# Kernel tuning notes

Hardware: AMD Instinct MI355X
Metric: run time of the kernel (lower is better)

Reference implementation:

```python
import jax, jax.numpy as jnp
import numpy as np

HIDDEN = 1024
NUM_HEADS = 16
B, S = 2, 2048


def _mha(x, w_in, b_in, w_out, b_out, num_heads):
    # x: [..., L, E]; standard nn.MultiheadAttention math (eval mode, no dropout)
    lead = x.shape[:-2]
    L, E = x.shape[-2], x.shape[-1]
    dh = E // num_heads
    qkv = x @ w_in.T + b_in                      # [..., L, 3E]
    q, k, v = jnp.split(qkv, 3, axis=-1)
    q = q.reshape(lead + (L, num_heads, dh)) * (dh ** -0.5)
    k = k.reshape(lead + (L, num_heads, dh))
    v = v.reshape(lead + (L, num_heads, dh))
    scores = jnp.einsum('...qhd,...khd->...hqk', q, k)
    probs = jax.nn.softmax(scores, axis=-1)
    out = jnp.einsum('...hqk,...khd->...qhd', probs, v).reshape(lead + (L, E))
    return out @ w_out.T + b_out


def setup_inputs() -> dict:
    key = jax.random.key(0)
    ks = jax.random.split(key, 12)
    E = HIDDEN
    s_in = 1.0 / np.sqrt(E)
    inp = {
        'x': jax.random.normal(ks[0], (B, S, E), dtype=jnp.float32),
        'w_in_g': jax.random.normal(ks[1], (3 * E, E), dtype=jnp.float32) * s_in,
        'b_in_g': jnp.zeros((3 * E,), dtype=jnp.float32),
        'w_out_g': jax.random.normal(ks[2], (E, E), dtype=jnp.float32) * s_in,
        'b_out_g': jnp.zeros((E,), dtype=jnp.float32),
        'w_in_l': jax.random.normal(ks[3], (3 * E, E), dtype=jnp.float32) * s_in,
        'b_in_l': jnp.zeros((3 * E,), dtype=jnp.float32),
        'w_out_l': jax.random.normal(ks[4], (E, E), dtype=jnp.float32) * s_in,
        'b_out_l': jnp.zeros((E,), dtype=jnp.float32),
        'w_f': jax.random.normal(ks[5], (E, 2 * E), dtype=jnp.float32) * (1.0 / np.sqrt(2 * E)),
        'b_f': jnp.zeros((E,), dtype=jnp.float32),
    }
    return inp


def reference(x, w_in_g, b_in_g, w_out_g, b_out_g,
              w_in_l, b_in_l, w_out_l, b_out_l, w_f, b_f):
    Bn, Sn, E = x.shape
    # global full attention over the whole sequence
    g = _mha(x, w_in_g, b_in_g, w_out_g, b_out_g, NUM_HEADS)   # [B,S,E]
    # block-local attention: blocks of length num_heads along the sequence
    sub_len = NUM_HEADS
    sub_num = Sn // sub_len
    xb = x.reshape(Bn, sub_num, sub_len, E)
    l = _mha(xb, w_in_l, b_in_l, w_out_l, b_out_l, NUM_HEADS).reshape(Bn, Sn, E)
    fused = jnp.concatenate([g, l], axis=-1)                   # [B,S,2E]
    return fused @ w_f.T + b_f
```

## Files before the change

### kernel.cpp

```cpp
#include <hip/hip_runtime.h>
#include <hip/hip_bf16.h>
#include <math.h>
#include <stdint.h>

constexpr int Bz = 2;
constexpr int S  = 2048;
constexpr int E  = 1024;
constexpr int NH = 16;
constexpr int DH = 64;
constexpr int QS = 6144;

typedef __attribute__((ext_vector_type(8))) short short8;
typedef __attribute__((ext_vector_type(4))) float f32x4;
typedef __attribute__((ext_vector_type(8))) unsigned short bf16x8;
typedef __attribute__((ext_vector_type(4))) unsigned short bf16x4;

__device__ __forceinline__ float bf2f(unsigned short u) {
    union { unsigned int i; float f; } c; c.i = ((unsigned int)u) << 16; return c.f;
}
__device__ __forceinline__ unsigned short f2bf(float f) {
    union { float f; unsigned int i; } c; c.f = f;
    unsigned int r = c.i + 0x7fffu + ((c.i >> 16) & 1u);
    return (unsigned short)(r >> 16);
}

__device__ __forceinline__ void pack4_store(unsigned short* dst,
                                            float a, float b, float c, float d) {
#if __has_builtin(__builtin_amdgcn_cvt_pk_bf16_f32)
    auto p0 = __builtin_amdgcn_cvt_pk_bf16_f32(a, b);
    auto p1 = __builtin_amdgcn_cvt_pk_bf16_f32(c, d);
    union { decltype(p0) v; unsigned int u; } c0, c1;
    c0.v = p0; c1.v = p1;
    uint2 w; w.x = c0.u; w.y = c1.u;
    *(uint2*)dst = w;
#else
    bf16x4 o = { f2bf(a), f2bf(b), f2bf(c), f2bf(d) };
    *(bf16x4*)dst = o;
#endif
}

#define GLD_LDS(g, l) __builtin_amdgcn_global_load_lds( \
    (const __attribute__((address_space(1))) void*)(g), \
    (__attribute__((address_space(3))) void*)(l), 16, 0, 0)

struct PrepArgs {
    const float* csrc[4]; unsigned short* cdst[4]; int cn[4];
    const float* wog; const float* wol;
    unsigned short* wogT; unsigned short* wolT;
    const float* wf; const float* bf; const float* bog; const float* bol;
    float* cb;
};

__global__ __launch_bounds__(256)
void prep_all(PrepArgs a)
{
    __shared__ unsigned short T[64][72];
    const int bid = blockIdx.x, t = threadIdx.x;

    if (bid < 12288) {
        int i = (bid * 256 + t) * 4;
        #pragma unroll
        for (int r = 0; r < 4; ++r) {
            if (i < a.cn[r]) {
                float4 v = *(const float4*)(a.csrc[r] + i);
                bf16x4 o = { f2bf(v.x), f2bf(v.y), f2bf(v.z), f2bf(v.w) };
                *(bf16x4*)(a.cdst[r] + i) = o;
                return;
            }
            i -= a.cn[r];
        }
        return;
    }
    if (bid < 12800) {
        const int id = bid - 12288;
        const int tj = id & 15, ti = (id >> 4) & 15, mat = id >> 8;
        const float* src = mat ? a.wol : a.wog;
        unsigned short* dst = mat ? a.wolT : a.wogT;
        #pragma unroll
        for (int r = 0; r < 4; ++r) {
            const int c = r * 256 + t;
            const int row = c >> 4, col4 = (c & 15) * 4;
            float4 v = *(const float4*)(src + (size_t)(ti * 64 + row) * 1024 + tj * 64 + col4);
            T[col4 + 0][row] = f2bf(v.x);
            T[col4 + 1][row] = f2bf(v.y);
            T[col4 + 2][row] = f2bf(v.z);
            T[col4 + 3][row] = f2bf(v.w);
        }
        __syncthreads();
        #pragma unroll
        for (int r = 0; r < 2; ++r) {
            const int c = r * 256 + t;
            const int jrow = c >> 3, ig = (c & 7) * 8;
            bf16x8 o;
            #pragma unroll
            for (int k = 0; k < 8; ++k) o[k] = T[jrow][ig + k];
            *(bf16x8*)(dst + (size_t)(tj * 64 + jrow) * 1024 + ti * 64 + ig) = o;
        }
        return;
    }
    {
        const int lane = t & 63;
        const int n = (bid - 12800) * 4 + (t >> 6);
        const float* row = a.wf + (size_t)n * 2048;
        float s = 0.f;
        #pragma unroll
        for (int i = 0; i < 16; ++i) s = fmaf(row[i * 64 + lane], a.bog[i * 64 + lane], s);
        #pragma unroll
        for (int i = 16; i < 32; ++i) s = fmaf(row[i * 64 + lane], a.bol[i * 64 + lane - 1024], s);
        #pragma unroll
        for (int off = 32; off > 0; off >>= 1) s += __shfl_xor(s, off, 64);
        if (lane == 0) a.cb[n] = a.bf[n] + s;
    }
}

struct GemmFusedArgs {
    const unsigned short* xb;    const unsigned short* win;
    const unsigned short* wfb;   const unsigned short* woutT;
    const float* bg;             const float* bl;
    unsigned short* qkv;  unsigned short* vt;  unsigned short* vtl;
    unsigned short* wcomb;
};

__global__ __launch_bounds__(256, 2)
void gemm_fused(GemmFusedArgs g)
{
    __shared__ __align__(16) short As[128 * 64];
    __shared__ __align__(16) short Bs[128 * 64];

    const int bid = blockIdx.x;
    const unsigned short *A, *W;
    unsigned short *C, *vt, *vtl;
    const float *bias0, *bias1;
    int m0, n0, lda, ldw, ldc, nsplit;

    if (bid < 1536) {
        m0 = (bid / 48) * 128;  n0 = (bid % 48) * 128;
        A = g.xb;  W = g.win;  C = g.qkv;  vt = g.vt;  vtl = g.vtl;
        bias0 = g.bg;  bias1 = g.bl;
        lda = 1024;  ldw = 1024;  ldc = QS;  nsplit = 3072;
    } else {
        const int id = bid - 1536;
        const int z = id >> 6;
        m0 = ((id >> 3) & 7) * 128;  n0 = (id & 7) * 128;
        A = g.wfb + z * 1024;
        W = g.woutT + (size_t)z * 1024 * 1024;
        C = g.wcomb + z * 1024;
        vt = nullptr;  vtl = nullptr;  bias0 = nullptr;  bias1 = nullptr;
        lda = 2048;  ldw = 1024;  ldc = 2048;  nsplit = 0;
    }

    const int t = threadIdx.x;
    const int lane = t & 63, wave = t >> 6;
    const int wm = wave & 1, wn = wave >> 1;
    const int lm = lane & 15, lk = lane >> 4;

    f32x4 acc[4][4] = {};

    const int row0 = t >> 3, kg0 = (t & 7) * 8;
    const unsigned short* a0 = A + (size_t)(m0 + row0) * lda + kg0;
    const unsigned short* w0 = W + (size_t)(n0 + row0) * ldw + kg0;

    for (int k0 = 0; k0 < 1024; k0 += 64) {
        __syncthreads();
        #pragma unroll
        for (int r = 0; r < 4; ++r)
            GLD_LDS(a0 + (size_t)(r * 32) * lda + k0, As + ((size_t)(r * 256 + wave * 64)) * 8);
        #pragma unroll
        for (int r = 0; r < 4; ++r)
            GLD_LDS(w0 + (size_t)(r * 32) * ldw + k0, Bs + ((size_t)(r * 256 + wave * 64)) * 8);
        __syncthreads();

        #pragma unroll
        for (int ks = 0; ks < 2; ++ks) {
            short8 af[4], bfr[4];
            #pragma unroll
            for (int i = 0; i < 4; ++i)
                af[i] = *(const short8*)&As[(wm * 64 + i * 16 + lm) * 64 + ks * 32 + lk * 8];
            #pragma unroll
            for (int j = 0; j < 4; ++j)
                bfr[j] = *(const short8*)&Bs[(wn * 64 + j * 16 + lm) * 64 + ks * 32 + lk * 8];
            #pragma unroll
            for (int i = 0; i < 4; ++i)
                #pragma unroll
                for (int j = 0; j < 4; ++j)
                    acc[i][j] = __builtin_amdgcn_mfma_f32_16x16x32_bf16(af[i], bfr[j], acc[i][j], 0, 0, 0);
        }
    }

    #pragma unroll
    for (int i = 0; i < 4; ++i) {
        #pragma unroll
        for (int j = 0; j < 4; ++j) {
            const int nn = n0 + wn * 64 + j * 16 + lm;
            const float bv = (nn < nsplit) ? (bias0 ? bias0[nn] : 0.f)
                                           : (bias1 ? bias1[nn - nsplit] : 0.f);
            const int mm0 = m0 + wm * 64 + i * 16 + lk * 4;
            float vv[4];
            #pragma unroll
            for (int r = 0; r < 4; ++r) {
                vv[r] = acc[i][j][r] + bv;
                C[(size_t)(mm0 + r) * ldc + nn] = f2bf(vv[r]);
            }
            if (vt) {
                const int nl = nn - 2048;
                if (nl >= 0 && nl < 1024) {
                    const int hh = nl >> 6, dd = nl & 63;
                    const int bb = mm0 >> 11, ss = mm0 & 2047;
                    pack4_store(vt + ((size_t)(bb * NH + hh) * 64 + dd) * S + ss,
                                vv[0], vv[1], vv[2], vv[3]);
                }
                const int nl2 = nn - 5120;
                if (nl2 >= 0) {
                    const int hh = nl2 >> 6, dd = nl2 & 63;
                    const int bb = mm0 >> 11, ss = mm0 & 2047;
                    pack4_store(vtl + ((size_t)(bb * NH + hh) * 64 + dd) * S + ss,
                                vv[0], vv[1], vv[2], vv[3]);
                }
            }
        }
    }
}

template<typename OutT>
__global__ __launch_bounds__(256, 2)
void gemm_m64(const unsigned short* __restrict__ A, const unsigned short* __restrict__ W,
              const float* __restrict__ bias, OutT* __restrict__ C,
              int M, int N, int K, int lda, int ldw, int ldc,
              size_t sAz, size_t sWz, size_t sCz)
{
    __shared__ __align__(16) short As[64 * 32];
    __shared__ __align__(16) short Bs[128 * 32];
    const int z = blockIdx.z;
    A += z * sAz;  W += z * sWz;  C += z * sCz;

    const int t = threadIdx.x;
    const int lane = t & 63, wave = t >> 6;
    const int wm = wave & 1, wn = wave >> 1;
    const int m0 = blockIdx.y * 64, n0 = blockIdx.x * 128;
    const int lm = lane & 15, lk = lane >> 4;

    f32x4 acc[2][4] = {};

    const int rowA = t >> 2, kgA = (t & 3) * 8;
    const unsigned short* aptr = A + (size_t)(m0 + rowA) * lda + kgA;
    const unsigned short* wptr = W + (size_t)(n0 + rowA) * ldw + kgA;

    for (int k0 = 0; k0 < K; k0 += 32) {
        __syncthreads();
        GLD_LDS(aptr + k0, As + ((size_t)(wave * 64)) * 8);
        #pragma unroll
        for (int r = 0; r < 2; ++r)
            GLD_LDS(wptr + (size_t)(r * 64) * ldw + k0, Bs + ((size_t)(r * 256 + wave * 64)) * 8);
        __syncthreads();

        short8 af[2], bfr[4];
        #pragma unroll
        for (int i = 0; i < 2; ++i)
            af[i] = *(const short8*)&As[(wm * 32 + i * 16 + lm) * 32 + lk * 8];
        #pragma unroll
        for (int j = 0; j < 4; ++j)
            bfr[j] = *(const short8*)&Bs[(wn * 64 + j * 16 + lm) * 32 + lk * 8];
        #pragma unroll
        for (int i = 0; i < 2; ++i)
            #pragma unroll
            for (int j = 0; j < 4; ++j)
                acc[i][j] = __builtin_amdgcn_mfma_f32_16x16x32_bf16(af[i], bfr[j], acc[i][j], 0, 0, 0);
    }

    #pragma unroll
    for (int i = 0; i < 2; ++i) {
        #pragma unroll
        for (int j = 0; j < 4; ++j) {
            const int nn = n0 + wn * 64 + j * 16 + lm;
            const float bv = bias ? bias[nn] : 0.f;
            #pragma unroll
            for (int r = 0; r < 4; ++r) {
                const int mm = m0 + wm * 32 + i * 16 + lk * 4 + r;
                const float v = acc[i][j][r] + bv;
                const size_t idx = (size_t)mm * ldc + nn;
                if constexpr (sizeof(OutT) == 2) ((unsigned short*)C)[idx] = f2bf(v);
                else                             C[idx] = v;
            }
        }
    }
}

__global__ __launch_bounds__(256, 2)
void attn_fused(const unsigned short* __restrict__ qkv,
                const unsigned short* __restrict__ vt,
                const unsigned short* __restrict__ vtl,
                unsigned short* __restrict__ attn)
{
    __shared__ __align__(16) unsigned short Ks[2][64][32];
    __shared__ __align__(16) unsigned short Vs[2][64][32];
    __shared__ __align__(16) unsigned short Pt[4][2][16][64];

    const int t = threadIdx.x, lane = t & 63, wq = t >> 6;
    const int lm = lane & 15, lk = lane >> 4;

    if (blockIdx.x < 512) {
        const int bid = blockIdx.x;
        const int qb = bid & 15;
        const int h  = (bid >> 4) & 15;
        const int b  = bid >> 8;
        const int q0 = qb * 128 + wq * 32;

        constexpr float QSCALE = 0.125f * 1.44269504088896340736f;
        short8 qf[2][2];
        #pragma unroll
        for (int qg = 0; qg < 2; ++qg) {
            const unsigned short* qrow = qkv + ((size_t)(b * S) + q0 + qg * 16 + lm) * QS + h * DH;
            #pragma unroll
            for (int kk = 0; kk < 2; ++kk) {
                bf16x8 v = *(const bf16x8*)(qrow + kk * 32 + lk * 8);
                #pragma unroll
                for (int j = 0; j < 8; ++j)
                    ((unsigned short*)&qf[qg][kk])[j] = f2bf(bf2f(v[j]) * QSCALE);
            }
        }

        short8 ones;
        #pragma unroll
        for (int j = 0; j < 8; ++j) ((unsigned short*)&ones)[j] = 0x3F80;

        const int row0 = t >> 2;
        const int sw0 = (row0 ^ (row0 >> 2)) & 3;
        const int g0 = ((t & 3) ^ sw0) * 8;
        const unsigned short* kg[2];
        const unsigned short* vg[2];
        #pragma unroll
        for (int r = 0; r < 2; ++r) {
            kg[r] = qkv + ((size_t)(b * S) + row0) * QS + E + h * 64 + r * 32 + g0;
            vg[r] = vt + ((size_t)(b * NH + h) * 64 + row0) * S + r * 32 + g0;
        }
        unsigned short* kl[2] = { &Ks[0][0][0] + (wq * 64) * 8, &Ks[0][0][0] + (256 + wq * 64) * 8 };
        unsigned short* vl[2] = { &Vs[0][0][0] + (wq * 64) * 8, &Vs[0][0][0] + (256 + wq * 64) * 8 };

        f32x4 O[2][4] = {};
        f32x4 lacc[2] = {};
        const int sw = lm & 7;
        const int fr = (lm ^ (lm >> 2)) & 3;

        for (int kt = 0; kt < 32; ++kt) {
            __syncthreads();
            GLD_LDS(kg[0] + (size_t)kt * 64 * QS, kl[0]);
            GLD_LDS(kg[1] + (size_t)kt * 64 * QS, kl[1]);
            GLD_LDS(vg[0] + kt * 64, vl[0]);
            GLD_LDS(vg[1] + kt * 64, vl[1]);
            __syncthreads();

            f32x4 st[2][4];
            #pragma unroll
            for (int qg = 0; qg < 2; ++qg)
                #pragma unroll
                for (int jn = 0; jn < 4; ++jn)
                    st[qg][jn] = (f32x4){ -16.f, -16.f, -16.f, -16.f };
            #pragma unroll
            for (int jn = 0; jn < 4; ++jn) {
                #pragma unroll
                for (int kk = 0; kk < 2; ++kk) {
                    short8 kf = *(const short8*)&Ks[kk][jn * 16 + lm][(lk ^ fr) * 8];
                    #pragma unroll
                    for (int qg = 0; qg < 2; ++qg)
                        st[qg][jn] = __builtin_amdgcn_mfma_f32_16x16x32_bf16(kf, qf[qg][kk], st[qg][jn], 0, 0, 0);
                }
            }

            #pragma unroll
            for (int qg = 0; qg < 2; ++qg)
                #pragma unroll
                for (int jn = 0; jn < 4; ++jn) {
                    const int cc = ((jn * 2 + (lk >> 1)) ^ sw) * 8 + (lk & 1) * 4;
                    pack4_store(&Pt[wq][qg][lm][cc],
                                exp2f(st[qg][jn][0]), exp2f(st[qg][jn][1]),
                                exp2f(st[qg][jn][2]), exp2f(st[qg][jn][3]));
                }

            short8 pf[2][2];
            #pragma unroll
            for (int qg = 0; qg < 2; ++qg) {
                pf[qg][0] = *(const short8*)&Pt[wq][qg][lm][((lk + 0) ^ sw) * 8];
                pf[qg][1] = *(const short8*)&Pt[wq][qg][lm][((lk + 4) ^ sw) * 8];
            }

            #pragma unroll
            for (int qg = 0; qg < 2; ++qg)
                #pragma unroll
                for (int kk = 0; kk < 2; ++kk)
                    lacc[qg] = __builtin_amdgcn_mfma_f32_16x16x32_bf16(ones, pf[qg][kk], lacc[qg], 0, 0, 0);

            #pragma unroll
            for (int jd = 0; jd < 4; ++jd) {
                #pragma unroll
                for (int kk = 0; kk < 2; ++kk) {
                    short8 vf = *(const short8*)&Vs[kk][jd * 16 + lm][(lk ^ fr) * 8];
                    #pragma unroll
                    for (int qg = 0; qg < 2; ++qg)
                        O[qg][jd] = __builtin_amdgcn_mfma_f32_16x16x32_bf16(vf, pf[qg][kk], O[qg][jd], 0, 0, 0);
                }
            }
        }

        #pragma unroll
        for (int qg = 0; qg < 2; ++qg) {
            const int q = q0 + qg * 16 + lm;
            const float inv = 1.0f / lacc[qg][0];
            unsigned short* dst = attn + ((size_t)(b * S) + q) * 2048 + h * 64 + lk * 4;
            #pragma unroll
            for (int jd = 0; jd < 4; ++jd)
                pack4_store(dst + jd * 16,
                            O[qg][jd][0] * inv, O[qg][jd][1] * inv,
                            O[qg][jd][2] * inv, O[qg][jd][3] * inv);
        }
        return;
    }

    unsigned short (*PtL)[16][32] = (unsigned short(*)[16][32])&Pt[0][0][0][0];
    const unsigned short* qkvl = qkv + 3072;
    const int gid = (blockIdx.x - 512) * 4 + wq;
    const int h   = gid & 15;
    const int sub = (gid >> 4) & 127;
    const int b   = gid >> 11;
    const int s0  = sub * 16;

    const unsigned short* base = qkvl + ((size_t)(b * S) + s0 + lm) * QS;
    f32x4 st = {};
    #pragma unroll
    for (int kk = 0; kk < 2; ++kk) {
        short8 kf = *(const short8*)(base + E + h * 64 + kk * 32 + lk * 8);
        short8 qf = *(const short8*)(base +     h * 64 + kk * 32 + lk * 8);
        st = __builtin_amdgcn_mfma_f32_16x16x32_bf16(kf, qf, st, 0, 0, 0);
    }

    constexpr float SC = 0.125f * 1.44269504088896340736f;
    float tt[4];
    #pragma unroll
    for (int r = 0; r < 4; ++r) tt[r] = st[r] * SC;
    float mx = fmaxf(fmaxf(tt[0], tt[1]), fmaxf(tt[2], tt[3]));
    mx = fmaxf(mx, __shfl_xor(mx, 16, 64));
    mx = fmaxf(mx, __shfl_xor(mx, 32, 64));
    float p[4], l = 0.f;
    #pragma unroll
    for (int r = 0; r < 4; ++r) { p[r] = exp2f(tt[r] - mx); l += p[r]; }
    l += __shfl_xor(l, 16, 64);
    l += __shfl_xor(l, 32, 64);
    const float inv = 1.0f / l;

    pack4_store(&PtL[wq][lm][lk * 4], p[0], p[1], p[2], p[3]);
    pack4_store(&PtL[wq][lm][16 + lk * 4], 0.f, 0.f, 0.f, 0.f);
    short8 pf = *(const short8*)&PtL[wq][lm][lk * 8];

    const unsigned short* vrow =
        vtl + (((size_t)(b * NH + h) * 64) + lm) * S + s0 + (lk & 1) * 8;
    f32x4 zero = {};
    unsigned short* dst = attn + ((size_t)(b * S) + s0 + lm) * 2048 + 1024 + h * 64 + lk * 4;
    #pragma unroll
    for (int jd = 0; jd < 4; ++jd) {
        short8 vf = *(const short8*)(vrow + (size_t)jd * 16 * S);
        f32x4 O = __builtin_amdgcn_mfma_f32_16x16x32_bf16(vf, pf, zero, 0, 0, 0);
        pack4_store(dst + jd * 16, O[0] * inv, O[1] * inv, O[2] * inv, O[3] * inv);
    }
}

extern "C" void kernel_launch(void* const* d_in, const int* in_sizes, int n_in,
                              void* d_out, int out_size, void* d_ws, size_t ws_size,
                              hipStream_t stream)
{
    const float* x       = (const float*)d_in[0];
    const float* w_in_g  = (const float*)d_in[1];
    const float* b_in_g  = (const float*)d_in[2];
    const float* w_out_g = (const float*)d_in[3];
    const float* b_out_g = (const float*)d_in[4];
    const float* w_in_l  = (const float*)d_in[5];
    const float* b_in_l  = (const float*)d_in[6];
    const float* w_out_l = (const float*)d_in[7];
    const float* b_out_l = (const float*)d_in[8];
    const float* w_f     = (const float*)d_in[9];
    const float* b_f     = (const float*)d_in[10];
    float* out = (float*)d_out;

    const int M = Bz * S;
    char* p = (char*)d_ws;
    unsigned short* xb       = (unsigned short*)p; p += (size_t)M * 1024 * 2;
    unsigned short* qkv_all  = (unsigned short*)p; p += (size_t)M * QS * 2;
    unsigned short* attn_cat = (unsigned short*)p; p += (size_t)M * 2048 * 2;
    unsigned short* win_all  = (unsigned short*)p; p += (size_t)6144 * 1024 * 2;
    unsigned short* wf_b     = (unsigned short*)p; p += (size_t)1024 * 2048 * 2;
    unsigned short* woutT    = (unsigned short*)p; p += (size_t)2 * 1024 * 1024 * 2;
    unsigned short* wcomb    = (unsigned short*)p; p += (size_t)1024 * 2048 * 2;
    unsigned short* vtbuf    = (unsigned short*)p; p += (size_t)Bz * NH * 64 * S * 2;
    unsigned short* vtlbuf   = (unsigned short*)p; p += (size_t)Bz * NH * 64 * S * 2;
    float*          cb       = (float*)p;          p += 1024 * 4;

    dim3 blk(256);

    PrepArgs pa;
    pa.csrc[0] = x;      pa.cdst[0] = xb;                    pa.cn[0] = M * 1024;
    pa.csrc[1] = w_in_g; pa.cdst[1] = win_all;               pa.cn[1] = 3072 * 1024;
    pa.csrc[2] = w_in_l; pa.cdst[2] = win_all + 3072 * 1024; pa.cn[2] = 3072 * 1024;
    pa.csrc[3] = w_f;    pa.cdst[3] = wf_b;                  pa.cn[3] = 1024 * 2048;
    pa.wog = w_out_g; pa.wol = w_out_l;
    pa.wogT = woutT;  pa.wolT = woutT + 1024 * 1024;
    pa.wf = w_f; pa.bf = b_f; pa.bog = b_out_g; pa.bol = b_out_l; pa.cb = cb;
    prep_all<<<dim3(13056), blk, 0, stream>>>(pa);

    GemmFusedArgs ga;
    ga.xb = xb;  ga.win = win_all;  ga.wfb = wf_b;  ga.woutT = woutT;
    ga.bg = b_in_g;  ga.bl = b_in_l;
    ga.qkv = qkv_all;  ga.vt = vtbuf;  ga.vtl = vtlbuf;  ga.wcomb = wcomb;
    gemm_fused<<<dim3(1664), blk, 0, stream>>>(ga);

    attn_fused<<<dim3(1536), blk, 0, stream>>>(qkv_all, vtbuf, vtlbuf, attn_cat);

    gemm_m64<float><<<dim3(1024 / 128, M / 64, 1), blk, 0, stream>>>(
        attn_cat, wcomb, cb, out,
        M, 1024, 2048, 2048, 2048, 1024,
        0, 0, 0);
}
```

Baseline: 291.7 us.

## Skip dead V stores, retile tail GEMM, remap attention blocks across XCDs

The fused QKV GEMM no longer writes the V columns to the row-major qkv buffer when they are already stored transposed, which saves write traffic. The final projection GEMM is replaced by a specialised kernel with 128x64 tiles and a 64-wide K step. That halves the number of barriers and raises MFMA work per LDS load. The global attention block index is also permuted so that blocks sharing a (batch, head) land on the same XCD, which should improve L2 reuse of K and V. This assumes nothing else reads the skipped V columns of qkv.

New measurement: 292.2 us (median of 3 runs). No clear change (+0.2%).

```diff
diff --git a/kernel.cpp b/kernel.cpp
--- a/kernel.cpp
+++ b/kernel.cpp
@@ -196,10 +196,11 @@
                                            : (bias1 ? bias1[nn - nsplit] : 0.f);
             const int mm0 = m0 + wm * 64 + i * 16 + lk * 4;
             float vv[4];
+            const bool deadC = vt && ((nn >= 2048 && nn < 3072) || nn >= 5120);
             #pragma unroll
             for (int r = 0; r < 4; ++r) {
                 vv[r] = acc[i][j][r] + bv;
-                C[(size_t)(mm0 + r) * ldc + nn] = f2bf(vv[r]);
+                if (!deadC) C[(size_t)(mm0 + r) * ldc + nn] = f2bf(vv[r]);
             }
             if (vt) {
                 const int nl = nn - 2048;
@@ -221,66 +222,62 @@
     }
 }
 
-template<typename OutT>
 __global__ __launch_bounds__(256, 2)
-void gemm_m64(const unsigned short* __restrict__ A, const unsigned short* __restrict__ W,
-              const float* __restrict__ bias, OutT* __restrict__ C,
-              int M, int N, int K, int lda, int ldw, int ldc,
-              size_t sAz, size_t sWz, size_t sCz)
+void gemm_tail(const unsigned short* __restrict__ A, const unsigned short* __restrict__ W,
+               const float* __restrict__ bias, float* __restrict__ C)
 {
-    __shared__ __align__(16) short As[64 * 32];
-    __shared__ __align__(16) short Bs[128 * 32];
-    const int z = blockIdx.z;
-    A += z * sAz;  W += z * sWz;  C += z * sCz;
+    __shared__ __align__(16) short As[128 * 64];
+    __shared__ __align__(16) short Bs[64 * 64];
 
     const int t = threadIdx.x;
     const int lane = t & 63, wave = t >> 6;
     const int wm = wave & 1, wn = wave >> 1;
-    const int m0 = blockIdx.y * 64, n0 = blockIdx.x * 128;
+    const int m0 = blockIdx.y * 128, n0 = blockIdx.x * 64;
     const int lm = lane & 15, lk = lane >> 4;
 
-    f32x4 acc[2][4] = {};
-
-    const int rowA = t >> 2, kgA = (t & 3) * 8;
-    const unsigned short* aptr = A + (size_t)(m0 + rowA) * lda + kgA;
-    const unsigned short* wptr = W + (size_t)(n0 + rowA) * ldw + kgA;
-
-    for (int k0 = 0; k0 < K; k0 += 32) {
+    f32x4 acc[4][2] = {};
+
+    const int row0 = t >> 3, kg0 = (t & 7) * 8;
+    const unsigned short* a0 = A + (size_t)(m0 + row0) * 2048 + kg0;
+    const unsigned short* w0 = W + (size_t)(n0 + row0) * 2048 + kg0;
+
+    for (int k0 = 0; k0 < 2048; k0 += 64) {
         __syncthreads();
-        GLD_LDS(aptr + k0, As + ((size_t)(wave * 64)) * 8);
+        #pragma unroll
+        for (int r = 0; r < 4; ++r)
+            GLD_LDS(a0 + (size_t)(r * 32) * 2048 + k0, As + ((size_t)(r * 256 + wave * 64)) * 8);
         #pragma unroll
         for (int r = 0; r < 2; ++r)
-            GLD_LDS(wptr + (size_t)(r * 64) * ldw + k0, Bs + ((size_t)(r * 256 + wave * 64)) * 8);
+            GLD_LDS(w0 + (size_t)(r * 32) * 2048 + k0, Bs + ((size_t)(r * 256 + wave * 64)) * 8);
         __syncthreads();
 
-        short8 af[2], bfr[4];
-        #pragma unroll
-        for (int i = 0; i < 2; ++i)
-            af[i] = *(const short8*)&As[(wm * 32 + i * 16 + lm) * 32 + lk * 8];
-        #pragma unroll
-        for (int j = 0; j < 4; ++j)
-            bfr[j] = *(const short8*)&Bs[(wn * 64 + j * 16 + lm) * 32 + lk * 8];
-        #pragma unroll
-        for (int i = 0; i < 2; ++i)
-            #pragma unroll
-            for (int j = 0; j < 4; ++j)
-                acc[i][j] = __builtin_amdgcn_mfma_f32_16x16x32_bf16(af[i], bfr[j], acc[i][j], 0, 0, 0);
+        #pragma unroll
+        for (int ks = 0; ks < 2; ++ks) {
+            short8 af[4], bfr[2];
+            #pragma unroll
+            for (int i = 0; i < 4; ++i)
+                af[i] = *(const short8*)&As[(wm * 64 + i * 16 + lm) * 64 + ks * 32 + lk * 8];
+            #pragma unroll
+            for (int j = 0; j < 2; ++j)
+                bfr[j] = *(const short8*)&Bs[(wn * 32 + j * 16 + lm) * 64 + ks * 32 + lk * 8];
+            #pragma unroll
+            for (int i = 0; i < 4; ++i)
+                #pragma unroll
+                for (int j = 0; j < 2; ++j)
+                    acc[i][j] = __builtin_amdgcn_mfma_f32_16x16x32_bf16(af[i], bfr[j], acc[i][j], 0, 0, 0);
+        }
     }
 
     #pragma unroll
-    for (int i = 0; i < 2; ++i) {
-        #pragma unroll
-        for (int j = 0; j < 4; ++j) {
-            const int nn = n0 + wn * 64 + j * 16 + lm;
-            const float bv = bias ? bias[nn] : 0.f;
-            #pragma unroll
-            for (int r = 0; r < 4; ++r) {
-                const int mm = m0 + wm * 32 + i * 16 + lk * 4 + r;
-                const float v = acc[i][j][r] + bv;
-                const size_t idx = (size_t)mm * ldc + nn;
-                if constexpr (sizeof(OutT) == 2) ((unsigned short*)C)[idx] = f2bf(v);
-                else                             C[idx] = v;
-            }
+    for (int i = 0; i < 4; ++i) {
+        #pragma unroll
+        for (int j = 0; j < 2; ++j) {
+            const int nn = n0 + wn * 32 + j * 16 + lm;
+            const float bv = bias[nn];
+            const int mm0 = m0 + wm * 64 + i * 16 + lk * 4;
+            #pragma unroll
+            for (int r = 0; r < 4; ++r)
+                C[(size_t)(mm0 + r) * 1024 + nn] = acc[i][j][r] + bv;
         }
     }
 }
@@ -300,9 +297,11 @@
 
     if (blockIdx.x < 512) {
         const int bid = blockIdx.x;
-        const int qb = bid & 15;
-        const int h  = (bid >> 4) & 15;
-        const int b  = bid >> 8;
+        const int slot = bid >> 3;
+        const int p  = (bid & 7) * 4 + (slot >> 4);
+        const int qb = slot & 15;
+        const int h  = p & 15;
+        const int b  = p >> 4;
         const int q0 = qb * 128 + wq * 32;
 
         constexpr float QSCALE = 0.125f * 1.44269504088896340736f;
@@ -512,8 +511,6 @@
 
     attn_fused<<<dim3(1536), blk, 0, stream>>>(qkv_all, vtbuf, vtlbuf, attn_cat);
 
-    gemm_m64<float><<<dim3(1024 / 128, M / 64, 1), blk, 0, stream>>>(
-        attn_cat, wcomb, cb, out,
-        M, 1024, 2048, 2048, 2048, 1024,
-        0, 0, 0);
-}
+    gemm_tail<<<dim3(1024 / 64, M / 128), blk, 0, stream>>>(
+        attn_cat, wcomb, cb, out);
+}
```
